# Kernel optimization log

Measured on AMD Instinct MI355X. Metric: run time of the kernel, lower is better.

## Reference

```python
import jax, jax.numpy as jnp
import numpy as np

EPS = 1e-8
FS = 10000
WIN_LEN = 256          # N_FRAME
HOP = WIN_LEN // 2     # 128
NFFT = 2 * WIN_LEN     # 512
NUMBAND = 15
MINFREQ = 150
N_INTEL = 30           # N, number of frames per intelligibility segment
BETA = -15.0
DYN_RANGE = 40.0


def _thirdoct(fs, nfft, num_bands, min_freq):
    """One-third octave band matrix (pystoi.utils.thirdoct)."""
    f = np.linspace(0, fs, nfft + 1)[: nfft // 2 + 1]
    k = np.arange(num_bands, dtype=np.float64)
    freq_low = min_freq * np.power(2.0, (2 * k - 1) / 6)
    freq_high = min_freq * np.power(2.0, (2 * k + 1) / 6)
    obm = np.zeros((num_bands, len(f)), dtype=np.float32)
    for i in range(num_bands):
        fl = int(np.argmin(np.square(f - freq_low[i])))
        fh = int(np.argmin(np.square(f - freq_high[i])))
        obm[i, fl:fh] = 1.0
    return obm


def _frame(x, framelen, hop):
    """x: (B, T) -> (B, nf, framelen) sliding frames (static index gather)."""
    T = x.shape[-1]
    nf = (T - framelen) // hop + 1
    idx = np.arange(framelen)[None, :] + hop * np.arange(nf)[:, None]
    return x[:, idx]


def _stoi(est, tgt, win, obm):
    B = tgt.shape[0]
    # ---- VAD: remove silent frames (stable-partition kept frames to front) ----
    xf = _frame(tgt, WIN_LEN, HOP) * win           # (B, nf, L)
    yf = _frame(est, WIN_LEN, HOP) * win
    energies = 20.0 * jnp.log10(jnp.linalg.norm(xf, axis=-1) + EPS)  # (B, nf)
    mask = (energies.max(-1, keepdims=True) - DYN_RANGE - energies) < 0
    nf = xf.shape[1]
    # stable argsort: kept (mask=True -> key 0) frames first, original order preserved
    order = jnp.argsort(jnp.logical_not(mask).astype(jnp.int32), axis=-1)
    xf = jnp.take_along_axis(xf, order[..., None], axis=1)
    yf = jnp.take_along_axis(yf, order[..., None], axis=1)
    counts = mask.sum(-1)                          # (B,) number of kept frames
    keep = (jnp.arange(nf)[None, :] < counts[:, None]).astype(xf.dtype)
    xf = xf * keep[..., None]
    yf = yf * keep[..., None]

    # ---- overlap-and-add (framelen == 2 * hop) -> (B, (nf+1)*HOP) ----
    def ola(fr):
        a = fr[:, :, :HOP].reshape(B, -1)
        b = fr[:, :, HOP:].reshape(B, -1)
        return jnp.pad(a, ((0, 0), (0, HOP))) + jnp.pad(b, ((0, 0), (HOP, 0)))

    x_sil = ola(xf)
    y_sil = ola(yf)

    # mask sorted descending then first element dropped -> ones at positions < count-1
    m = (jnp.arange(nf - 1)[None, :] < (counts[:, None] - 1)).astype(xf.dtype)  # (B, nf-1)

    # ---- STFT via framing + rfft (last frame dropped, as in module) ----
    def stft(x):
        fr = _frame(x, WIN_LEN, HOP)[:, :-1] * win        # (B, nf-1, L)
        return jnp.fft.rfft(fr, n=NFFT, axis=-1)          # (B, nf-1, F)

    x_spec = stft(x_sil) * m[..., None]
    y_spec = stft(y_sil) * m[..., None]

    # ---- one-third octave band energies ----
    x_tob = jnp.sqrt(jnp.einsum('kf,bnf->bkn', obm, jnp.abs(x_spec) ** 2) + EPS)
    y_tob = jnp.sqrt(jnp.einsum('kf,bnf->bkn', obm, jnp.abs(y_spec) ** 2) + EPS)

    # ---- N_INTEL-frame segments (unfold) ----
    n_stft = x_tob.shape[-1]
    M = n_stft - N_INTEL + 1
    sidx = np.arange(N_INTEL)[:, None] + np.arange(M)[None, :]
    x_seg = x_tob[:, :, sidx]                      # (B, K, N, M)
    y_seg = y_tob[:, :, sidx]
    m2 = m[:, N_INTEL - 1:]                        # (B, M)
    x_seg = x_seg * m2[:, None, None, :]
    y_seg = y_seg * m2[:, None, None, :]

    # ---- clipped, normalized correlation (non-extended STOI) ----
    norm_const = jnp.linalg.norm(x_seg, axis=2, keepdims=True) / (
        jnp.linalg.norm(y_seg, axis=2, keepdims=True) + EPS)
    clip_val = 10.0 ** (-BETA / 20.0)
    y_prim = jnp.minimum(y_seg * norm_const, x_seg * (1.0 + clip_val))
    y_prim = y_prim - y_prim.mean(2, keepdims=True)
    x_c = x_seg - x_seg.mean(2, keepdims=True)
    y_prim = y_prim / (jnp.linalg.norm(y_prim, axis=2, keepdims=True) + EPS)
    x_c = x_c / (jnp.linalg.norm(x_c, axis=2, keepdims=True) + EPS)
    corr = (y_prim * x_c).sum(2).mean(1)           # (B, M)
    out = corr.sum(-1) / (m2.sum(-1) + EPS)        # (B,)
    return -out


def setup_inputs() -> dict:
    key = jax.random.key(0)
    k1, k2 = jax.random.split(key)
    B, T = 32, 320000
    targets = jax.random.normal(k1, (B, T), dtype=jnp.float32)
    est_targets = targets + 0.3 * jax.random.normal(k2, (B, T), dtype=jnp.float32)
    win = jnp.asarray(np.hanning(WIN_LEN + 2)[1:-1], dtype=jnp.float32)
    obm = jnp.asarray(_thirdoct(FS, NFFT, NUMBAND, MINFREQ))
    return {"est_targets": est_targets, "targets": targets, "win": win, "obm": obm}


def reference(est_targets, targets, win, obm):
    return _stoi(est_targets, targets, win, obm)
```

## Files before the change

### kernel.cpp

```cpp
#include <hip/hip_runtime.h>
#include <math.h>

#define EPSF 1e-8f
#define WIN_LEN 256
#define HOP 128
#define NBINS 257
#define NUMBAND 15
#define NFRAMES 2499
#define NSTFT 2498
#define N_INTEL 30
#define NSEG 2469
#define NB 32
#define T_LEN 320000
#define CLIP_VAL 5.623413251903491f
#define NHALF 2500
#define AB_STRIDE 2560

typedef float v2f __attribute__((ext_vector_type(2)));
typedef float v4f __attribute__((ext_vector_type(4)));

__device__ __forceinline__ void pk_fma_blo(v2f& d, v2f a, v2f b) {
    asm("v_pk_fma_f32 %0, %1, %2, %0 op_sel:[0,0,0] op_sel_hi:[1,0,1]"
        : "+v"(d) : "v"(a), "v"(b));
}
__device__ __forceinline__ void pk_fma_rot(v2f& d, v2f a, v2f b) {
    asm("v_pk_fma_f32 %0, %1, %2, %0 op_sel:[1,1,0] op_sel_hi:[0,1,1] neg_lo:[1,0,0]"
        : "+v"(d) : "v"(a), "v"(b));
}
__device__ __forceinline__ void pk_fma_nbhi(v2f& d, v2f a, v2f b) {
    asm("v_pk_fma_f32 %0, %1, %2, %0 op_sel:[0,1,0] op_sel_hi:[1,1,1] neg_lo:[1,0,0] neg_hi:[1,0,0]"
        : "+v"(d) : "v"(a), "v"(b));
}
__device__ __forceinline__ void pk_fma_s(v2f& d, v2f a, float s) {
    const v2f bv = { s, s };
    asm("v_pk_fma_f32 %0, %1, %2, %0"
        : "+v"(d) : "v"(a), "v"(bv));
}
__device__ __forceinline__ v2f pk_mul_blo(v2f a, v2f b) {
    v2f d;
    asm("v_pk_mul_f32 %0, %1, %2 op_sel:[0,0] op_sel_hi:[1,0]"
        : "=v"(d) : "v"(a), "v"(b));
    return d;
}
__device__ __forceinline__ v2f pk_mul_bhi(v2f a, v2f b) {
    v2f d;
    asm("v_pk_mul_f32 %0, %1, %2 op_sel:[0,1] op_sel_hi:[1,1]"
        : "=v"(d) : "v"(a), "v"(b));
    return d;
}
__device__ __forceinline__ v2f pk_mul_s(v2f a, float s) {
    const v2f bv = { s, s };
    v2f d;
    asm("v_pk_mul_f32 %0, %1, %2" : "=v"(d) : "v"(a), "v"(bv));
    return d;
}
__device__ __forceinline__ v2f pk_add(v2f a, v2f b) {
    v2f d;
    asm("v_pk_add_f32 %0, %1, %2" : "=v"(d) : "v"(a), "v"(b));
    return d;
}
__device__ __forceinline__ v2f pk_sub(v2f a, v2f b) {
    v2f d;
    asm("v_pk_add_f32 %0, %1, %2 neg_lo:[0,1] neg_hi:[0,1]" : "=v"(d) : "v"(a), "v"(b));
    return d;
}
__device__ __forceinline__ v2f pk_bmi(v2f B, v2f D) {
    v2f d;
    asm("v_pk_add_f32 %0, %1, %2 op_sel:[1,0] op_sel_hi:[0,1] neg_hi:[1,0]"
        : "=v"(d) : "v"(D), "v"(B));
    return d;
}
__device__ __forceinline__ v2f pk_bpi(v2f B, v2f D) {
    v2f d;
    asm("v_pk_add_f32 %0, %1, %2 op_sel:[1,0] op_sel_hi:[0,1] neg_lo:[1,0]"
        : "=v"(d) : "v"(D), "v"(B));
    return d;
}
__device__ __forceinline__ v2f pk_cmul(v2f a, v2f b) {
    v2f t;
    asm("v_pk_mul_f32 %0, %1, %2 op_sel:[0,0] op_sel_hi:[1,0]"
        : "=v"(t) : "v"(a), "v"(b));
    asm("v_pk_fma_f32 %0, %1, %2, %0 op_sel:[1,1,0] op_sel_hi:[0,1,1] neg_lo:[1,0,0]"
        : "+v"(t) : "v"(a), "v"(b));
    return t;
}
__device__ __forceinline__ void pk_rot(v2f& cs, v2f cksk) {
    v2f t;
    asm("v_pk_mul_f32 %0, %1, %2 op_sel:[0,0] op_sel_hi:[1,0]"
        : "=v"(t) : "v"(cs), "v"(cksk));
    asm("v_pk_fma_f32 %0, %0, %1, %2 op_sel:[1,1,0] op_sel_hi:[0,1,1] neg_lo:[1,0,0]"
        : "+v"(cs) : "v"(cksk), "v"(t));
}
__device__ __forceinline__ void pk_cfma(v2f& acc, v2f g, float wr, float wi) {
    const v2f wv = { wr, wi };
    pk_fma_blo(acc, g, wv);
    pk_fma_rot(acc, g, wv);
}

#define WS_COUNTS   0
#define WS_BANDLO   512
#define WS_BANDHI   768
#define WS_SRCFRM   5632
#define WS_XTOB     325632
#define WS_YTOB     5121792

__global__ __launch_bounds__(256)
void k1a_ab(const float* __restrict__ tgt, const float* __restrict__ win,
            const float* __restrict__ obm, float2* __restrict__ ab,
            int* __restrict__ band_lo, int* __restrict__ band_hi,
            float* __restrict__ out_)
{
    const int b = blockIdx.x;
    const int tid = threadIdx.x;
    const int h = blockIdx.y * 256 + tid;
    if (h < NHALF) {
        const float* xp = tgt + (size_t)b * T_LEN + (size_t)h * HOP;
        float sa = 0.f, sb = 0.f;
        #pragma unroll 4
        for (int u = 0; u < HOP; u += 4) {
            const float4 xv = *(const float4*)(xp + u);
            const float4 wl = *(const float4*)(win + u);
            const float4 wh = *(const float4*)(win + HOP + u);
            float a;
            a = xv.x * wl.x; sa = fmaf(a, a, sa);
            a = xv.y * wl.y; sa = fmaf(a, a, sa);
            a = xv.z * wl.z; sa = fmaf(a, a, sa);
            a = xv.w * wl.w; sa = fmaf(a, a, sa);
            a = xv.x * wh.x; sb = fmaf(a, a, sb);
            a = xv.y * wh.y; sb = fmaf(a, a, sb);
            a = xv.z * wh.z; sb = fmaf(a, a, sb);
            a = xv.w * wh.w; sb = fmaf(a, a, sb);
        }
        ab[(size_t)b * AB_STRIDE + h] = make_float2(sa, sb);
    }

    if (b == 0 && blockIdx.y == 0) {
        if (tid < NUMBAND) {
            int lo = -1, hi = 0;
            for (int k = 0; k < NBINS; ++k) {
                if (obm[tid * NBINS + k] != 0.f) { if (lo < 0) lo = k; hi = k + 1; }
            }
            band_lo[tid] = (lo < 0) ? 0 : lo;
            band_hi[tid] = hi;
        }
        __syncthreads();
        if (tid == 0) {
            int lo = NBINS, hi = 0;
            for (int i = 0; i < NUMBAND; ++i) {
                if (band_lo[i] < lo) lo = band_lo[i];
                if (band_hi[i] > hi) hi = band_hi[i];
            }
            band_lo[NUMBAND] = lo;
            band_hi[NUMBAND] = hi;
        }
        if (tid < NB) out_[tid] = 0.f;
    }
}

__global__ __launch_bounds__(256)
void k1b_scan(const float2* __restrict__ ab,
              int* __restrict__ counts, int* __restrict__ srcfrm)
{
    const int b = blockIdx.x;
    const int tid = threadIdx.x;
    __shared__ float nr[NFRAMES];
    __shared__ float red[256];
    __shared__ int   sc[256];

    const float2* abp = ab + (size_t)b * AB_STRIDE;
    for (int f = tid; f < NFRAMES; f += 256) {
        const float2 p0 = abp[f];
        const float2 p1 = abp[f + 1];
        nr[f] = sqrtf(p0.x + p1.y);
    }
    __syncthreads();

    float mx = 0.f;
    for (int f = tid; f < NFRAMES; f += 256) mx = fmaxf(mx, nr[f]);
    red[tid] = mx;
    __syncthreads();
    for (int s = 128; s > 0; s >>= 1) {
        if (tid < s) red[tid] = fmaxf(red[tid], red[tid + s]);
        __syncthreads();
    }
    const float thr = (red[0] + EPSF) * 0.01f;

    const int c0 = tid * 10;
    const int c1 = (c0 + 10 < NFRAMES) ? c0 + 10 : NFRAMES;
    int lc = 0;
    for (int f = c0; f < c1; ++f) if (nr[f] + EPSF > thr) ++lc;
    sc[tid] = lc;
    __syncthreads();
    #pragma unroll
    for (int off = 1; off < 256; off <<= 1) {
        int u = (tid >= off) ? sc[tid - off] : 0;
        __syncthreads();
        sc[tid] += u;
        __syncthreads();
    }
    if (tid == 0) counts[b] = sc[255];
    int pos = sc[tid] - lc;
    int* sf = srcfrm + b * NFRAMES;
    for (int f = c0; f < c1; ++f) if (nr[f] + EPSF > thr) sf[pos++] = f;
}

__global__ __launch_bounds__(64)
void k2_stft_tob(const float* __restrict__ est, const float* __restrict__ tgt,
                 const float* __restrict__ win,
                 const int* __restrict__ counts, const int* __restrict__ srcfrm,
                 const int* __restrict__ band_lo, const int* __restrict__ band_hi,
                 float* __restrict__ xtob, float* __restrict__ ytob)
{
    const int lin = blockIdx.x;
    const int xcd = lin & 7, cidx = lin >> 3;
    const int q = NSTFT >> 3, r = NSTFT & 7;
    const int j = (xcd < r ? xcd * (q + 1) : r * (q + 1) + (xcd - r) * q) + cidx;

    const int b = blockIdx.y;
    const int cntb = counts[b];
    if (j >= cntb - 1) return;

    const int tid = threadIdx.x;
    __shared__ float frf[512];
    __shared__ float sxr[2 * 16 * 68];

    const int* sf = srcfrm + b * NFRAMES;
    const float* xg = tgt + (size_t)b * T_LEN;
    const float* yg = est + (size_t)b * T_LEN;

    {
        const int t4 = 4 * tid;
        const int k0 = sf[j];
        const v4f wa = *(const v4f*)&win[t4];
        v4f xv, yv;
        if (tid < 32) {
            xv = *(const v4f*)&xg[k0 * HOP + t4] * wa;
            yv = *(const v4f*)&yg[k0 * HOP + t4] * wa;
            if (j >= 1) {
                const int km = sf[j - 1];
                const v4f wb = *(const v4f*)&win[HOP + t4];
                xv += *(const v4f*)&xg[km * HOP + HOP + t4] * wb;
                yv += *(const v4f*)&yg[km * HOP + HOP + t4] * wb;
            }
        } else {
            const int kp = sf[j + 1];
            const v4f wb = *(const v4f*)&win[t4 - HOP];
            xv = *(const v4f*)&xg[k0 * HOP + t4] * wa
               + *(const v4f*)&xg[kp * HOP + t4 - HOP] * wb;
            yv = *(const v4f*)&yg[k0 * HOP + t4] * wa
               + *(const v4f*)&yg[kp * HOP + t4 - HOP] * wb;
        }
        xv *= wa; yv *= wa;
        const v4f lo = { xv.x, yv.x, xv.y, yv.y };
        const v4f hi = { xv.z, yv.z, xv.w, yv.w };
        *(v4f*)&frf[2 * t4]     = lo;
        *(v4f*)&frf[2 * t4 + 4] = hi;
    }
    __syncthreads();

    {
        const int m = tid & 3;
        const int c = tid >> 2;
        const float ke = (m == 0) ? 1.f : (m == 2) ? -1.f : 0.f;
        const float ki = (m == 1) ? -1.f : (m == 3) ? 1.f : 0.f;
        const float ang = -0.19634954084936207f * (float)m;
        const v2f cksk = { __cosf(ang), __sinf(ang) };
        v2f cs = { 1.f, 0.f };
        v2f URe[8], UIm[8];
        #pragma unroll
        for (int rr = 0; rr < 8; ++rr) {
            const v2f za = *(const v2f*)&frf[2 * (16 * rr + c)];
            const v2f zb = *(const v2f*)&frf[2 * (16 * rr + 128 + c)];
            v2f pre_re = za; pk_fma_s(pre_re, zb, ke);
            const v2f pre_im = pk_mul_s(zb, ki);
            v2f ur = pk_mul_blo(pre_re, cs); pk_fma_nbhi(ur, pre_im, cs);
            v2f ui = pk_mul_bhi(pre_re, cs); pk_fma_blo(ui, pre_im, cs);
            URe[rr] = ur; UIm[rr] = ui;
            pk_rot(cs, cksk);
        }
        v2f ARe[8], AIm[8];
        {
            const float C2 = 0.70710678118654752f;
            v2f dR, dI;
            #pragma unroll
            for (int rr = 0; rr < 4; ++rr) {
                ARe[rr] = pk_add(URe[rr], URe[rr + 4]);
                AIm[rr] = pk_add(UIm[rr], UIm[rr + 4]);
            }
            ARe[4] = pk_sub(URe[0], URe[4]);     AIm[4] = pk_sub(UIm[0], UIm[4]);
            dR = pk_sub(URe[1], URe[5]); dI = pk_sub(UIm[1], UIm[5]);
            ARe[5] = pk_mul_s(pk_add(dR, dI), C2);
            AIm[5] = pk_mul_s(pk_sub(dI, dR), C2);
            dR = pk_sub(URe[2], URe[6]); dI = pk_sub(UIm[2], UIm[6]);
            ARe[6] = dI;                         AIm[6] = pk_mul_s(dR, -1.f);
            dR = pk_sub(URe[3], URe[7]); dI = pk_sub(UIm[3], UIm[7]);
            ARe[7] = pk_mul_s(pk_sub(dI, dR), C2);
            AIm[7] = pk_mul_s(pk_add(dR, dI), -C2);
        }
        v2f BRe[8], BIm[8];
        #pragma unroll
        for (int g = 0; g < 8; g += 4) {
            BRe[g + 0] = pk_add(ARe[g + 0], ARe[g + 2]);  BIm[g + 0] = pk_add(AIm[g + 0], AIm[g + 2]);
            BRe[g + 1] = pk_add(ARe[g + 1], ARe[g + 3]);  BIm[g + 1] = pk_add(AIm[g + 1], AIm[g + 3]);
            BRe[g + 2] = pk_sub(ARe[g + 0], ARe[g + 2]);  BIm[g + 2] = pk_sub(AIm[g + 0], AIm[g + 2]);
            const v2f dR = pk_sub(ARe[g + 1], ARe[g + 3]);
            const v2f dI = pk_sub(AIm[g + 1], AIm[g + 3]);
            BRe[g + 3] = dI;  BIm[g + 3] = pk_mul_s(dR, -1.f);
        }
        const int kmap[8] = { 0, 4, 2, 6, 1, 5, 3, 7 };
        #pragma unroll
        for (int p = 0; p < 8; ++p) {
            const int pb = p & ~1;
            v2f oR, oI;
            if (p & 1) { oR = pk_sub(BRe[pb], BRe[pb + 1]); oI = pk_sub(BIm[pb], BIm[pb + 1]); }
            else       { oR = pk_add(BRe[pb], BRe[pb + 1]); oI = pk_add(BIm[pb], BIm[pb + 1]); }
            const int mj = m + 4 * kmap[p];
            *(v2f*)&sxr[c * 68 + mj * 2]        = (v2f){ oR.x, oI.x };
            *(v2f*)&sxr[1088 + c * 68 + mj * 2] = (v2f){ oR.y, oI.y };
        }
    }
    __syncthreads();

    const int blo = band_lo[NUMBAND];
    const int base = blo & ~31;
    float* px = frf;
    float* py = frf + 224;
    {
        const int m2 = tid & 31;
        const int sig = tid >> 5;
        const float* sbase = sxr + sig * 1088 + m2 * 2;
        const float ang = -0.012271846303085130f * (float)(base + m2);
        const v2f cksk = { __cosf(ang), __sinf(ang) };
        v2f cs = { 1.f, 0.f };
        v2f V[16];
        #pragma unroll
        for (int t0 = 0; t0 < 16; ++t0) {
            const v2f s = *(const v2f*)(sbase + t0 * 68);
            V[t0] = (t0 == 0) ? s : pk_cmul(cs, s);
            pk_rot(cs, cksk);
        }
        v2f G[4][4];
        #pragma unroll
        for (int rr = 0; rr < 4; ++rr) {
            const v2f A = pk_add(V[rr], V[rr + 8]);
            const v2f B = pk_sub(V[rr], V[rr + 8]);
            const v2f C = pk_add(V[rr + 4], V[rr + 12]);
            const v2f D = pk_sub(V[rr + 4], V[rr + 12]);
            G[0][rr] = pk_add(A, C);
            G[2][rr] = pk_sub(A, C);
            G[1][rr] = pk_bmi(B, D);
            G[3][rr] = pk_bpi(B, D);
        }
        float* pout = sig ? py : px;
        #define C1 0.92387953251f
        #define S1 0.38268343236f
        #define C2c 0.70710678119f
        {
            const v2f a_ = pk_add(pk_add(G[0][0], G[0][1]), pk_add(G[0][2], G[0][3]));
            pout[0 * 32 + m2] = fmaf(a_.x, a_.x, a_.y * a_.y);
        }
        #define XOUT(P, D, W1R, W1I, W2R, W2I, W3R, W3I) { \
            v2f a_ = G[D][0]; \
            pk_cfma(a_, G[D][1], W1R, W1I); \
            pk_cfma(a_, G[D][2], W2R, W2I); \
            pk_cfma(a_, G[D][3], W3R, W3I); \
            pout[(P) * 32 + m2] = fmaf(a_.x, a_.x, a_.y * a_.y); }
        XOUT(1, 1,  C1, -S1,     C2c, -C2c,   S1, -C1)
        XOUT(2, 2,  C2c, -C2c,   0.f, -1.f,  -C2c, -C2c)
        XOUT(3, 3,  S1, -C1,    -C2c, -C2c,  -C1,  S1)
        {
            const v2f t1_ = pk_sub(G[0][0], G[0][2]);
            const v2f t2_ = pk_sub(G[0][1], G[0][3]);
            const v2f a_ = pk_bmi(t1_, t2_);
            pout[4 * 32 + m2] = fmaf(a_.x, a_.x, a_.y * a_.y);
        }
        XOUT(5, 1, -S1, -C1,    -C2c,  C2c,   C1,  S1)
        XOUT(6, 2, -C2c, -C2c,   0.f,  1.f,   C2c, -C2c)
        #undef XOUT
    }
    __syncthreads();

    if (tid < 4 * NUMBAND) {
        const int band = tid >> 2, s = tid & 3;
        const int lop = band_lo[band] - base, hip = band_hi[band] - base;
        const int u0 = lop >> 1, ul = (hip - 1) >> 1;
        float sx = 0.f, sy = 0.f;
        for (int u = u0 + s; u <= ul; u += 4) {
            const v2f pvx = *(const v2f*)&px[2 * u];
            const v2f pvy = *(const v2f*)&py[2 * u];
            const float m0 = (2 * u >= lop) ? 1.f : 0.f;
            const float m1 = (2 * u + 1 < hip) ? 1.f : 0.f;
            sx = fmaf(m0, pvx.x, sx); sx = fmaf(m1, pvx.y, sx);
            sy = fmaf(m0, pvy.x, sy); sy = fmaf(m1, pvy.y, sy);
        }
        sx += __shfl_xor(sx, 1, 64);  sx += __shfl_xor(sx, 2, 64);
        sy += __shfl_xor(sy, 1, 64);  sy += __shfl_xor(sy, 2, 64);
        if (s == 0) {
            xtob[((size_t)b * NUMBAND + band) * NSTFT + j] = sqrtf(sx + EPSF);
            ytob[((size_t)b * NUMBAND + band) * NSTFT + j] = sqrtf(sy + EPSF);
        }
    }
}

__global__ __launch_bounds__(256)
void k3_corr(const float* __restrict__ xtob, const float* __restrict__ ytob,
             const int* __restrict__ counts, float* __restrict__ out_)
{
    const int bb = blockIdx.y;
    const int b = bb / NUMBAND;
    const int band = bb % NUMBAND;
    const int s_base = blockIdx.x * 256;
    const int tid = threadIdx.x;
    const int seg = s_base + tid;

    __shared__ v2f lxy[256 + N_INTEL - 1];
    const float* xr = xtob + ((size_t)b * NUMBAND + band) * NSTFT;
    const float* yr = ytob + ((size_t)b * NUMBAND + band) * NSTFT;
    for (int i = tid; i < 256 + N_INTEL - 1; i += 256) {
        const int g = s_base + i;
        v2f v = { 0.f, 0.f };
        if (g < NSTFT) v = (v2f){ xr[g], yr[g] };
        lxy[i] = v;
    }
    __syncthreads();

    int nvalid = counts[b] - N_INTEL;
    if (nvalid < 0) nvalid = 0;
    if (nvalid > NSEG) nvalid = NSEG;

    float d = 0.f;
    if (seg < nvalid) {
        float xv[N_INTEL], yv[N_INTEL];
        float sx2 = 0.f, sy2 = 0.f;
        #pragma unroll
        for (int i = 0; i < N_INTEL; ++i) {
            const v2f v = lxy[tid + i];
            xv[i] = v.x; yv[i] = v.y;
            sx2 = fmaf(xv[i], xv[i], sx2);
            sy2 = fmaf(yv[i], yv[i], sy2);
        }
        const float nc = sqrtf(sx2) / (sqrtf(sy2) + EPSF);
        float sy = 0.f, sx = 0.f;
        #pragma unroll
        for (int i = 0; i < N_INTEL; ++i) {
            const float yp = fminf(yv[i] * nc, xv[i] * (1.f + CLIP_VAL));
            yv[i] = yp;
            sy += yp; sx += xv[i];
        }
        const float my = sy * (1.f / N_INTEL);
        const float mxm = sx * (1.f / N_INTEL);
        float num = 0.f, dy = 0.f, dx2 = 0.f;
        #pragma unroll
        for (int i = 0; i < N_INTEL; ++i) {
            const float a = yv[i] - my;
            const float c = xv[i] - mxm;
            num = fmaf(a, c, num);
            dy  = fmaf(a, a, dy);
            dx2 = fmaf(c, c, dx2);
        }
        d = num / ((sqrtf(dy) + EPSF) * (sqrtf(dx2) + EPSF));
    }

    #pragma unroll
    for (int o = 32; o > 0; o >>= 1) d += __shfl_down(d, o, 64);
    __shared__ float wsum[4];
    const int lane = threadIdx.x & 63, wid = threadIdx.x >> 6;
    if (lane == 0) wsum[wid] = d;
    __syncthreads();
    if (threadIdx.x == 0) {
        const float scale = -1.f / ((float)NUMBAND * ((float)nvalid + EPSF));
        atomicAdd(&out_[b], (wsum[0] + wsum[1] + wsum[2] + wsum[3]) * scale);
    }
}

extern "C" void kernel_launch(void* const* d_in, const int* in_sizes, int n_in,
                              void* d_out, int out_size, void* d_ws, size_t ws_size,
                              hipStream_t stream) {
    (void)in_sizes; (void)n_in; (void)out_size; (void)ws_size;
    const float* est = (const float*)d_in[0];
    const float* tgt = (const float*)d_in[1];
    const float* win = (const float*)d_in[2];
    const float* obm = (const float*)d_in[3];
    float* out = (float*)d_out;

    char* ws = (char*)d_ws;
    int*   counts  = (int*)(ws + WS_COUNTS);
    int*   band_lo = (int*)(ws + WS_BANDLO);
    int*   band_hi = (int*)(ws + WS_BANDHI);
    int*   srcfrm  = (int*)(ws + WS_SRCFRM);
    float* xtob    = (float*)(ws + WS_XTOB);
    float* ytob    = (float*)(ws + WS_YTOB);
    float2* ab     = (float2*)xtob;

    k1a_ab<<<dim3(NB, 10), dim3(256), 0, stream>>>(tgt, win, obm, ab,
                                                   band_lo, band_hi, out);
    k1b_scan<<<dim3(NB), dim3(256), 0, stream>>>(ab, counts, srcfrm);
    k2_stft_tob<<<dim3(NSTFT, NB), dim3(64), 0, stream>>>(est, tgt, win, counts, srcfrm,
                                                          band_lo, band_hi, xtob, ytob);
    k3_corr<<<dim3((NSEG + 255) / 256, NB * NUMBAND), dim3(256), 0, stream>>>(xtob, ytob,
                                                                              counts, out);
}
```

Before: 186.0 us.

## Process two STFT frames per block and store intermediate FFT data as fp16

The STFT kernel now runs two frames per 128-thread block, one wavefront each, which halves the grid size. Invalid frames no longer return early; they compute with zeroed input and skip only the final write. The intermediate complex values between the two FFT stages are packed to fp16 in shared memory, which cuts LDS footprint and traffic. The fp16 storage loses precision in the spectrum, and invalid frames now spend compute that was previously skipped.

```diff
diff --git a/kernel.cpp b/kernel.cpp
--- a/kernel.cpp
+++ b/kernel.cpp
@@ -15,6 +15,7 @@
 #define CLIP_VAL 5.623413251903491f
 #define NHALF 2500
 #define AB_STRIDE 2560
+#define NWX 1249
 
 typedef float v2f __attribute__((ext_vector_type(2)));
 typedef float v4f __attribute__((ext_vector_type(4)));
@@ -95,6 +96,17 @@
     const v2f wv = { wr, wi };
     pk_fma_blo(acc, g, wv);
     pk_fma_rot(acc, g, wv);
+}
+__device__ __forceinline__ unsigned pk_f16(float a, float b) {
+    unsigned u;
+    asm("v_cvt_pkrtz_f16_f32 %0, %1, %2" : "=v"(u) : "v"(a), "v"(b));
+    return u;
+}
+__device__ __forceinline__ v2f unpk_f16(unsigned u) {
+    float lo, hi;
+    asm("v_cvt_f32_f16 %0, %1" : "=v"(lo) : "v"(u));
+    asm("v_lshrrev_b32 %0, 16, %1\n\tv_cvt_f32_f16 %0, %0" : "=v"(hi) : "v"(u));
+    return (v2f){ lo, hi };
 }
 
 #define WS_COUNTS   0
@@ -204,7 +216,7 @@
     for (int f = c0; f < c1; ++f) if (nr[f] + EPSF > thr) sf[pos++] = f;
 }
 
-__global__ __launch_bounds__(64)
+__global__ __launch_bounds__(128)
 void k2_stft_tob(const float* __restrict__ est, const float* __restrict__ tgt,
                  const float* __restrict__ win,
                  const int* __restrict__ counts, const int* __restrict__ srcfrm,
@@ -213,16 +225,19 @@
 {
     const int lin = blockIdx.x;
     const int xcd = lin & 7, cidx = lin >> 3;
-    const int q = NSTFT >> 3, r = NSTFT & 7;
-    const int j = (xcd < r ? xcd * (q + 1) : r * (q + 1) + (xcd - r) * q) + cidx;
+    const int q = NWX >> 3, r = NWX & 7;
+    const int rl = (xcd < r ? xcd * (q + 1) : r * (q + 1) + (xcd - r) * q) + cidx;
+
+    const int wave = threadIdx.x >> 6;
+    const int tid = threadIdx.x & 63;
+    const int j = rl * 2 + wave;
 
     const int b = blockIdx.y;
     const int cntb = counts[b];
-    if (j >= cntb - 1) return;
-
-    const int tid = threadIdx.x;
-    __shared__ float frf[512];
-    __shared__ float sxr[2 * 16 * 68];
+    const bool valid = (j < cntb - 1);
+
+    __shared__ float    frf[2][512];
+    __shared__ unsigned sxh[2][2][16][34];
 
     const int* sf = srcfrm + b * NFRAMES;
     const float* xg = tgt + (size_t)b * T_LEN;
@@ -230,31 +245,33 @@
 
     {
         const int t4 = 4 * tid;
-        const int k0 = sf[j];
+        v4f xv = { 0.f, 0.f, 0.f, 0.f }, yv = xv;
         const v4f wa = *(const v4f*)&win[t4];
-        v4f xv, yv;
-        if (tid < 32) {
-            xv = *(const v4f*)&xg[k0 * HOP + t4] * wa;
-            yv = *(const v4f*)&yg[k0 * HOP + t4] * wa;
-            if (j >= 1) {
-                const int km = sf[j - 1];
-                const v4f wb = *(const v4f*)&win[HOP + t4];
-                xv += *(const v4f*)&xg[km * HOP + HOP + t4] * wb;
-                yv += *(const v4f*)&yg[km * HOP + HOP + t4] * wb;
+        if (valid) {
+            const int k0 = sf[j];
+            if (tid < 32) {
+                xv = *(const v4f*)&xg[k0 * HOP + t4] * wa;
+                yv = *(const v4f*)&yg[k0 * HOP + t4] * wa;
+                if (j >= 1) {
+                    const int km = sf[j - 1];
+                    const v4f wb = *(const v4f*)&win[HOP + t4];
+                    xv += *(const v4f*)&xg[km * HOP + HOP + t4] * wb;
+                    yv += *(const v4f*)&yg[km * HOP + HOP + t4] * wb;
+                }
+            } else {
+                const int kp = sf[j + 1];
+                const v4f wb = *(const v4f*)&win[t4 - HOP];
+                xv = *(const v4f*)&xg[k0 * HOP + t4] * wa
+                   + *(const v4f*)&xg[kp * HOP + t4 - HOP] * wb;
+                yv = *(const v4f*)&yg[k0 * HOP + t4] * wa
+                   + *(const v4f*)&yg[kp * HOP + t4 - HOP] * wb;
             }
-        } else {
-            const int kp = sf[j + 1];
-            const v4f wb = *(const v4f*)&win[t4 - HOP];
-            xv = *(const v4f*)&xg[k0 * HOP + t4] * wa
-               + *(const v4f*)&xg[kp * HOP + t4 - HOP] * wb;
-            yv = *(const v4f*)&yg[k0 * HOP + t4] * wa
-               + *(const v4f*)&yg[kp * HOP + t4 - HOP] * wb;
         }
         xv *= wa; yv *= wa;
         const v4f lo = { xv.x, yv.x, xv.y, yv.y };
         const v4f hi = { xv.z, yv.z, xv.w, yv.w };
-        *(v4f*)&frf[2 * t4]     = lo;
-        *(v4f*)&frf[2 * t4 + 4] = hi;
+        *(v4f*)&frf[wave][2 * t4]     = lo;
+        *(v4f*)&frf[wave][2 * t4 + 4] = hi;
     }
     __syncthreads();
 
@@ -269,8 +286,8 @@
         v2f URe[8], UIm[8];
         #pragma unroll
         for (int rr = 0; rr < 8; ++rr) {
-            const v2f za = *(const v2f*)&frf[2 * (16 * rr + c)];
-            const v2f zb = *(const v2f*)&frf[2 * (16 * rr + 128 + c)];
+            const v2f za = *(const v2f*)&frf[wave][2 * (16 * rr + c)];
+            const v2f zb = *(const v2f*)&frf[wave][2 * (16 * rr + 128 + c)];
             v2f pre_re = za; pk_fma_s(pre_re, zb, ke);
             const v2f pre_im = pk_mul_s(zb, ki);
             v2f ur = pk_mul_blo(pre_re, cs); pk_fma_nbhi(ur, pre_im, cs);
@@ -315,27 +332,26 @@
             if (p & 1) { oR = pk_sub(BRe[pb], BRe[pb + 1]); oI = pk_sub(BIm[pb], BIm[pb + 1]); }
             else       { oR = pk_add(BRe[pb], BRe[pb + 1]); oI = pk_add(BIm[pb], BIm[pb + 1]); }
             const int mj = m + 4 * kmap[p];
-            *(v2f*)&sxr[c * 68 + mj * 2]        = (v2f){ oR.x, oI.x };
-            *(v2f*)&sxr[1088 + c * 68 + mj * 2] = (v2f){ oR.y, oI.y };
+            sxh[wave][0][c][mj] = pk_f16(oR.x, oI.x);
+            sxh[wave][1][c][mj] = pk_f16(oR.y, oI.y);
         }
     }
     __syncthreads();
 
     const int blo = band_lo[NUMBAND];
     const int base = blo & ~31;
-    float* px = frf;
-    float* py = frf + 224;
+    float* px = frf[wave];
+    float* py = frf[wave] + 224;
     {
         const int m2 = tid & 31;
         const int sig = tid >> 5;
-        const float* sbase = sxr + sig * 1088 + m2 * 2;
         const float ang = -0.012271846303085130f * (float)(base + m2);
         const v2f cksk = { __cosf(ang), __sinf(ang) };
         v2f cs = { 1.f, 0.f };
         v2f V[16];
         #pragma unroll
         for (int t0 = 0; t0 < 16; ++t0) {
-            const v2f s = *(const v2f*)(sbase + t0 * 68);
+            const v2f s = unpk_f16(sxh[wave][sig][t0][m2]);
             V[t0] = (t0 == 0) ? s : pk_cmul(cs, s);
             pk_rot(cs, cksk);
         }
@@ -380,7 +396,7 @@
     }
     __syncthreads();
 
-    if (tid < 4 * NUMBAND) {
+    if (tid < 4 * NUMBAND && valid) {
         const int band = tid >> 2, s = tid & 3;
         const int lop = band_lo[band] - base, hip = band_hi[band] - base;
         const int u0 = lop >> 1, ul = (hip - 1) >> 1;
@@ -495,8 +511,8 @@
     k1a_ab<<<dim3(NB, 10), dim3(256), 0, stream>>>(tgt, win, obm, ab,
                                                    band_lo, band_hi, out);
     k1b_scan<<<dim3(NB), dim3(256), 0, stream>>>(ab, counts, srcfrm);
-    k2_stft_tob<<<dim3(NSTFT, NB), dim3(64), 0, stream>>>(est, tgt, win, counts, srcfrm,
-                                                          band_lo, band_hi, xtob, ytob);
+    k2_stft_tob<<<dim3(NWX, NB), dim3(128), 0, stream>>>(est, tgt, win, counts, srcfrm,
+                                                         band_lo, band_hi, xtob, ytob);
     k3_corr<<<dim3((NSEG + 255) / 256, NB * NUMBAND), dim3(256), 0, stream>>>(xtob, ytob,
                                                                               counts, out);
 }
```

After: 173.0 us. 7.0% less time.
